# Optimization experiments

Measured on AMD Instinct MI355X. Metric: run time of the kernel, lower is better.

## Reference

```python
import jax, jax.numpy as jnp
import numpy as np


def sparse_conv3d(images, kernel, default_value, base_plane, dilations=(1, 1, 1)):
    """Sparse 3D conv over a per-pixel base-plane-aligned volume.

    images:     [B, H, W, D, C]  local depth slabs per pixel
    kernel:     [kh, kw, kd, C, F]
    base_plane: [B, H, W, 1] int  global depth offset of slab start per pixel
    Neighbor sample at pixel (h', w') and local depth d uses that neighbor's
    local index d + od + base_plane[h,w] - base_plane[h',w']; out-of-range
    (spatial or depth) samples are filled with default_value.
    """
    B, H, W, D, C = images.shape
    kh, kw, kd, _, F = kernel.shape
    d0, d1, d2 = dilations
    bp = base_plane[..., 0].astype(jnp.int32)  # [B,H,W]
    hs = jnp.arange(H)
    ws = jnp.arange(W)
    ds = jnp.arange(D)
    dv = jnp.asarray(default_value, images.dtype).reshape(())
    out = jnp.zeros((B, H, W, D, F), images.dtype)
    for i in range(kh):
        oh = (i - kh // 2) * d0
        h_idx = hs + oh
        valid_h = (h_idx >= 0) & (h_idx < H)
        h_c = jnp.clip(h_idx, 0, H - 1)
        for j in range(kw):
            ow = (j - kw // 2) * d1
            w_idx = ws + ow
            valid_w = (w_idx >= 0) & (w_idx < W)
            w_c = jnp.clip(w_idx, 0, W - 1)
            # gather shifted neighbor slabs and their base offsets
            img_n = images[:, h_c][:, :, w_c]      # [B,H,W,D,C]
            bp_n = bp[:, h_c][:, :, w_c]            # [B,H,W]
            rel = (bp - bp_n)[..., None]            # depth realignment [B,H,W,1]
            sp_valid = (valid_h[None, :, None, None] & valid_w[None, None, :, None])
            for k in range(kd):
                od = (k - kd // 2) * d2
                d_idx = ds[None, None, None, :] + od + rel  # [B,H,W,D]
                valid = sp_valid & (d_idx >= 0) & (d_idx < D)
                d_c = jnp.clip(d_idx, 0, D - 1)
                vals = jnp.take_along_axis(img_n, d_c[..., None], axis=3)  # [B,H,W,D,C]
                vals = jnp.where(valid[..., None], vals, dv)
                out = out + jnp.einsum('bhwdc,cf->bhwdf', vals, kernel[i, j, k])
    return out


def setup_inputs() -> dict:
    key = jax.random.key(0)
    k1, k2, k3 = jax.random.split(key, 3)
    B, H, W, D, C, F = 2, 96, 128, 32, 16, 16
    images = jax.random.normal(k1, (B, H, W, D, C), dtype=jnp.float32)
    base_plane = jax.random.randint(k2, (B, H, W, 1), 0, 8, dtype=jnp.int32)
    kernel = jax.random.normal(k3, (3, 3, 3, C, F), dtype=jnp.float32) * 0.05
    default_value = jnp.zeros((1,), dtype=jnp.float32)
    return {"images": images, "base_plane": base_plane, "kernel": kernel,
            "default_value": default_value}


def reference(images, base_plane, kernel, default_value):
    return sparse_conv3d(images, kernel, default_value[0], base_plane, dilations=(1, 1, 1))
```

## Files before the change

kernel.cpp:

```cpp
#include <hip/hip_runtime.h>
#include <hip/hip_bf16.h>

typedef __attribute__((ext_vector_type(8))) short short8;
typedef __attribute__((ext_vector_type(4))) short s16x4;
typedef __attribute__((ext_vector_type(4))) float f32x4;

#define NB_H 96
#define NB_W 128
#define NB_D 32
#define NB_C 16
#define NB_F 16
#define NPIX (2 * NB_H * NB_W)
#define KB2_U16 (14 * 512)
#define WS_NEED ((size_t)KB2_U16 * 2)
#define SLAB_STRIDE 1280
#define NSLAB 24
#define DV_OFF (NSLAB * SLAB_STRIDE)
#define LDS_BYTES (DV_OFF + 64)

static __device__ __forceinline__ short fcvt(float f) {
  return (short)__builtin_bit_cast(unsigned short, __float2bfloat16(f));
}


__global__ __launch_bounds__(256) void sconv3d_wprep(
    const float* __restrict__ kern, unsigned short* __restrict__ kb2) {
  const int i = blockIdx.x * 256 + threadIdx.x;
  if (i >= KB2_U16) return;
  const int p = i >> 9;
  const int g = (i >> 7) & 3;
  const int f = (i >> 3) & 15;
  const int j = i & 7;
  const int k = g * 8 + j;
  int lo, hi;
  if (p < 12) {
    const int q = p / 3, m = p % 3;
    lo = (m == 0) ? 6 * q : (m == 1) ? 6 * q + 3 : 6 * q + 2;
    hi = (m == 0) ? 6 * q + 1 : (m == 1) ? 6 * q + 4 : 6 * q + 5;
  } else if (p == 12) { lo = 24; hi = 25; }
  else { lo = 26; hi = -1; }
  const int t = (k < 16) ? lo : hi;
  const int c = k & 15;
  kb2[i] = (t >= 0) ? (unsigned short)fcvt(kern[(t * 16 + c) * 16 + f])
                    : (unsigned short)0;
}

__global__ __launch_bounds__(256, 4) void sconv3d_fused4(
    const float* __restrict__ img, const int* __restrict__ bp,
    const unsigned short* __restrict__ kb2, const float* __restrict__ dvp,
    float* __restrict__ out) {
  __shared__ char Sb[LDS_BYTES];
  const int tid = threadIdx.x;
  const int lane = tid & 63;
  const int r = lane & 15;
  const int grp = lane >> 4;
  const int vc = (grp & 1) * 16;
  const int halfbit = grp >> 1;
  const int rA = r + halfbit - 1;
  const int rX = r + 1;
  const int voff_dv = DV_OFF + vc;

  short8 bfrag[14];
#pragma unroll
  for (int p = 0; p < 14; ++p)
    bfrag[p] = *(const short8*)(kb2 + p * 512 + grp * 128 + r * 8);

  const int bid = (blockIdx.x & 7) * 384 + (blockIdx.x >> 3);
  const int b = bid >= 1536;
  const int rem = bid - b * 1536;
  const int h0 = (rem >> 5) * 2;
  const int w0 = (rem & 31) * 4;

  const int t2 = tid & 127;
  const int sg = tid >> 7;
  const int srow = t2 >> 2;
  const int sb8 = (t2 & 3) * 8;
#pragma unroll
  for (int pass = 0; pass < 12; ++pass) {
    const int s = pass * 2 + sg;
    const int dh = s / 6, dw = s - 6 * dh;
    const int hh = min(max(h0 + dh - 1, 0), NB_H - 1);
    const int ww = min(max(w0 + dw - 1, 0), NB_W - 1);
    const float4 v = *(const float4*)(
        img + ((b * NB_H + hh) * NB_W + ww) * (NB_D * NB_C) + t2 * 4);
    s16x4 o;
    o[0] = fcvt(v.x); o[1] = fcvt(v.y); o[2] = fcvt(v.z); o[3] = fcvt(v.w);
    *(s16x4*)(Sb + s * SLAB_STRIDE + srow * 40 + sb8) = o;
  }
  if (tid < 16) ((unsigned short*)(Sb + DV_OFF))[tid] =
      (unsigned short)fcvt(dvp[0]);

  const int wid = __builtin_amdgcn_readfirstlane((int)(tid >> 6));
  const int w = w0 + wid;
  const int hA = h0, hB = h0 + 1;
  const int pixA = (b * NB_H + hA) * NB_W + w;
  const int pixB = pixA + NB_W;
  const int bpcA = bp[pixA];
  const int bpcB = bp[pixB];

#define CALCN(PH, H, BPC, DI, DJ, SV, BA, RE)                           \
  {                                                                     \
    const int hh = (H) + (DI), ww = w + (DJ);                           \
    SV = (hh >= 0) & (hh < NB_H) & (ww >= 0) & (ww < NB_W);             \
    const int hc = min(max(hh, 0), NB_H - 1);                           \
    const int wc = min(max(ww, 0), NB_W - 1);                           \
    RE = (BPC)-bp[(b * NB_H + hc) * NB_W + wc];                         \
    BA = (((PH) + (DI) + 1) * 6 + wid + (DJ) + 1) * SLAB_STRIDE;        \
  }

  int Asv0, Aba0, Are0, Asv1, Aba1, Are1, Asv2, Aba2, Are2;
  int Asv3, Aba3, Are3, Asv4, Aba4, Are4, Asv5, Aba5, Are5;
  int Asv6, Aba6, Are6, Asv7, Aba7, Are7, Asv8, Aba8, Are8;
  int Bsv0, Bba0, Bre0, Bsv1, Bba1, Bre1, Bsv2, Bba2, Bre2;
  int Bsv3, Bba3, Bre3, Bsv4, Bba4, Bre4, Bsv5, Bba5, Bre5;
  int Bsv6, Bba6, Bre6, Bsv7, Bba7, Bre7, Bsv8, Bba8, Bre8;
  CALCN(0, hA, bpcA, -1, -1, Asv0, Aba0, Are0);
  CALCN(0, hA, bpcA, -1, 0, Asv1, Aba1, Are1);
  CALCN(0, hA, bpcA, -1, 1, Asv2, Aba2, Are2);
  CALCN(0, hA, bpcA, 0, -1, Asv3, Aba3, Are3);
  CALCN(0, hA, bpcA, 0, 0, Asv4, Aba4, Are4);
  CALCN(0, hA, bpcA, 0, 1, Asv5, Aba5, Are5);
  CALCN(0, hA, bpcA, 1, -1, Asv6, Aba6, Are6);
  CALCN(0, hA, bpcA, 1, 0, Asv7, Aba7, Are7);
  CALCN(0, hA, bpcA, 1, 1, Asv8, Aba8, Are8);
  CALCN(1, hB, bpcB, -1, -1, Bsv0, Bba0, Bre0);
  CALCN(1, hB, bpcB, -1, 0, Bsv1, Bba1, Bre1);
  CALCN(1, hB, bpcB, -1, 1, Bsv2, Bba2, Bre2);
  CALCN(1, hB, bpcB, 0, -1, Bsv3, Bba3, Bre3);
  CALCN(1, hB, bpcB, 0, 0, Bsv4, Bba4, Bre4);
  CALCN(1, hB, bpcB, 0, 1, Bsv5, Bba5, Bre5);
  CALCN(1, hB, bpcB, 1, -1, Bsv6, Bba6, Bre6);
  CALCN(1, hB, bpcB, 1, 0, Bsv7, Bba7, Bre7);
  CALCN(1, hB, bpcB, 1, 1, Bsv8, Bba8, Bre8);
#undef CALCN

  __syncthreads();

  f32x4 accA0 = {0.f, 0.f, 0.f, 0.f}, accA1 = {0.f, 0.f, 0.f, 0.f};
  f32x4 accB0 = {0.f, 0.f, 0.f, 0.f}, accB1 = {0.f, 0.f, 0.f, 0.f};

  short8 Xa0, Xa1, Xb0, Xb1, Ya0, Ya1, Yb0, Yb1;

#define LOADQ(S, DS0A, BAA, SVA, DS0B, BAB, SVB)                        \
  {                                                                     \
    int d_, o_;                                                         \
    d_ = (DS0A);      o_ = (BAA) + d_ * 40 + vc;                        \
    o_ = ((SVA) && (unsigned)d_ < NB_D) ? o_ : voff_dv;                 \
    S##a0 = *(const short8*)(Sb + o_);                                  \
    d_ = (DS0A) + 16; o_ = (BAA) + d_ * 40 + vc;                        \
    o_ = ((SVA) && (unsigned)d_ < NB_D) ? o_ : voff_dv;                 \
    S##a1 = *(const short8*)(Sb + o_);                                  \
    d_ = (DS0B);      o_ = (BAB) + d_ * 40 + vc;                        \
    o_ = ((SVB) && (unsigned)d_ < NB_D) ? o_ : voff_dv;                 \
    S##b0 = *(const short8*)(Sb + o_);                                  \
    d_ = (DS0B) + 16; o_ = (BAB) + d_ * 40 + vc;                        \
    o_ = ((SVB) && (unsigned)d_ < NB_D) ? o_ : voff_dv;                 \
    S##b1 = *(const short8*)(Sb + o_);                                  \
  }

#define LOAD_U(S, N) \
  LOADQ(S, rA + Are##N, Aba##N, Asv##N, rA + Bre##N, Bba##N, Bsv##N)

#define LOAD_M(S, NE, NO)                                               \
  {                                                                     \
    const int asv = halfbit ? Asv##NO : Asv##NE;                        \
    const int aba = halfbit ? Aba##NO : Aba##NE;                        \
    const int are = halfbit ? Are##NO : Are##NE;                        \
    const int bsv = halfbit ? Bsv##NO : Bsv##NE;                        \
    const int bba = halfbit ? Bba##NO : Bba##NE;                        \
    const int bre = halfbit ? Bre##NO : Bre##NE;                        \
    LOADQ(S, rX + are, aba, asv, rX + bre, bba, bsv)                    \
  }

#define LOAD_M13(S, NE)                                                 \
  {                                                                     \
    const int asv = halfbit ? 0 : Asv##NE;                              \
    const int bsv = halfbit ? 0 : Bsv##NE;                              \
    LOADQ(S, rX + Are##NE, Aba##NE, asv, rX + Bre##NE, Bba##NE, bsv)    \
  }

#define FMA4(P, S)                                                      \
  {                                                                     \
    const short8 bf = bfrag[P];                                         \
    accA0 = __builtin_amdgcn_mfma_f32_16x16x32_bf16(S##a0, bf, accA0, 0, 0, 0); \
    accA1 = __builtin_amdgcn_mfma_f32_16x16x32_bf16(S##a1, bf, accA1, 0, 0, 0); \
    accB0 = __builtin_amdgcn_mfma_f32_16x16x32_bf16(S##b0, bf, accB0, 0, 0, 0); \
    accB1 = __builtin_amdgcn_mfma_f32_16x16x32_bf16(S##b1, bf, accB1, 0, 0, 0); \
  }

  LOAD_U(X, 0);
  LOAD_U(Y, 1);
  FMA4(0, X);  LOAD_M(X, 0, 1);
  FMA4(1, Y);  LOAD_U(Y, 2);
  FMA4(2, X);  LOAD_U(X, 3);
  FMA4(3, Y);  LOAD_M(Y, 2, 3);
  FMA4(4, X);  LOAD_U(X, 4);
  FMA4(5, Y);  LOAD_U(Y, 5);
  FMA4(6, X);  LOAD_M(X, 4, 5);
  FMA4(7, Y);  LOAD_U(Y, 6);
  FMA4(8, X);  LOAD_U(X, 7);
  FMA4(9, Y);  LOAD_M(Y, 6, 7);
  FMA4(10, X); LOAD_U(X, 8);
  FMA4(11, Y); LOAD_M13(Y, 8);
  FMA4(12, X);
  FMA4(13, Y);

#undef LOADQ
#undef LOAD_U
#undef LOAD_M
#undef LOAD_M13
#undef FMA4

  const int obaseA = pixA * (NB_D * NB_F);
  const int obaseB = pixB * (NB_D * NB_F);
#pragma unroll
  for (int rr = 0; rr < 4; ++rr) {
    out[obaseA + (grp * 4 + rr) * NB_F + r] = accA0[rr];
    out[obaseA + (grp * 4 + rr + 16) * NB_F + r] = accA1[rr];
    out[obaseB + (grp * 4 + rr) * NB_F + r] = accB0[rr];
    out[obaseB + (grp * 4 + rr + 16) * NB_F + r] = accB1[rr];
  }
}

__global__ __launch_bounds__(256) void sconv3d_mfma(
    const float* __restrict__ img, const int* __restrict__ bp,
    const float* __restrict__ kern, const float* __restrict__ dvp,
    float* __restrict__ out, int npix) {
  __shared__ unsigned short Kb[28 * 256];
  const int tid = threadIdx.x;
  for (int idx = tid; idx < 28 * 256; idx += 256) {
    unsigned short v = 0;
    if (idx < 27 * 256) v = (unsigned short)fcvt(kern[idx]);
    Kb[idx] = v;
  }
  __syncthreads();

  const int lane = tid & 63;
  const int grp = lane >> 4;
  const int r = lane & 15;
  const int c0 = (grp & 1) * 8;
  const int half = grp >> 1;

  short8 bfrag[14];
#pragma unroll
  for (int p = 0; p < 14; ++p) {
#pragma unroll
    for (int j = 0; j < 8; ++j) {
      const int k = 8 * grp + j;
      const int t = 2 * p + (k >> 4);
      bfrag[p][j] = (short)Kb[t * 256 + (k & 15) * 16 + r];
    }
  }

  const int pix = blockIdx.x * 4 + (tid >> 6);
  if (pix >= npix) return;
  const int b = pix / (NB_H * NB_W);
  const int rem = pix - b * (NB_H * NB_W);
  const int h = rem >> 7;
  const int w = rem & (NB_W - 1);

  const float dv = dvp[0];
  const int bpc = bp[pix];

  f32x4 acc0 = {0.f, 0.f, 0.f, 0.f};
  f32x4 acc1 = {0.f, 0.f, 0.f, 0.f};

#pragma unroll
  for (int p = 0; p < 14; ++p) {
    const int t = 2 * p + half;
    const int n = t / 3;
    const int kd = t - 3 * n;
    const int i = n / 3;
    const int j = n - 3 * i;
    const int hh = h + i - 1;
    const int ww = w + j - 1;
    const bool sv =
        (t < 27) && (hh >= 0) && (hh < NB_H) && (ww >= 0) && (ww < NB_W);
    const int hc = min(max(hh, 0), NB_H - 1);
    const int wc = min(max(ww, 0), NB_W - 1);
    const int nidx = (b * NB_H + hc) * NB_W + wc;
    const int rel = bpc - bp[nidx];
    const int base = nidx * (NB_D * NB_C);
    const int dsh = (kd - 1) + rel;

    const int ds0 = r + dsh;
    short8 a0;
    {
      float va[8];
      if (sv && (ds0 >= 0) && (ds0 < NB_D)) {
        const float4* pp = (const float4*)(img + base + ds0 * NB_C + c0);
        const float4 x = pp[0];
        const float4 y = pp[1];
        va[0] = x.x; va[1] = x.y; va[2] = x.z; va[3] = x.w;
        va[4] = y.x; va[5] = y.y; va[6] = y.z; va[7] = y.w;
      } else {
#pragma unroll
        for (int q = 0; q < 8; ++q) va[q] = dv;
      }
#pragma unroll
      for (int q = 0; q < 8; ++q) a0[q] = fcvt(va[q]);
    }
    acc0 = __builtin_amdgcn_mfma_f32_16x16x32_bf16(a0, bfrag[p], acc0, 0, 0, 0);

    const int ds1 = ds0 + 16;
    short8 a1;
    {
      float va[8];
      if (sv && (ds1 >= 0) && (ds1 < NB_D)) {
        const float4* pp = (const float4*)(img + base + ds1 * NB_C + c0);
        const float4 x = pp[0];
        const float4 y = pp[1];
        va[0] = x.x; va[1] = x.y; va[2] = x.z; va[3] = x.w;
        va[4] = y.x; va[5] = y.y; va[6] = y.z; va[7] = y.w;
      } else {
#pragma unroll
        for (int q = 0; q < 8; ++q) va[q] = dv;
      }
#pragma unroll
      for (int q = 0; q < 8; ++q) a1[q] = fcvt(va[q]);
    }
    acc1 = __builtin_amdgcn_mfma_f32_16x16x32_bf16(a1, bfrag[p], acc1, 0, 0, 0);
  }

  const int obase = pix * (NB_D * NB_F);
#pragma unroll
  for (int rr = 0; rr < 4; ++rr) {
    out[obase + (grp * 4 + rr) * NB_F + r] = acc0[rr];
    out[obase + (grp * 4 + rr + 16) * NB_F + r] = acc1[rr];
  }
}

extern "C" void kernel_launch(void* const* d_in, const int* in_sizes, int n_in,
                              void* d_out, int out_size, void* d_ws, size_t ws_size,
                              hipStream_t stream) {
  const float* img = (const float*)d_in[0];
  const int* bp = (const int*)d_in[1];
  const float* kern = (const float*)d_in[2];
  const float* dvp = (const float*)d_in[3];
  float* out = (float*)d_out;

  if (ws_size >= WS_NEED) {
    unsigned short* kb2 = (unsigned short*)d_ws;
    sconv3d_wprep<<<28, 256, 0, stream>>>(kern, kb2);
    sconv3d_fused4<<<NPIX / 8, 256, 0, stream>>>(img, bp, kb2, dvp, out);
  } else {
    sconv3d_mfma<<<NPIX / 4, 256, 0, stream>>>(img, bp, kern, dvp, out, NPIX);
  }
}
```

Measured before the change: 47.17 us.

## Roll a six-row LDS ring buffer so each block sweeps twelve output rows

Each block now covers a 12x4 pixel strip instead of 2x4. It keeps a rolling ring of six halo rows of bf16 slabs in LDS, and each step prefetches the next two rows into registers, overlapping those loads with the MFMA work on the current two rows. This cuts the redundant halo reloads from global memory (previously 24 slabs per 8 pixels) and spreads the weight-fragment setup over more work. In exchange the grid shrinks to 512 blocks with a larger LDS footprint and occupancy hint 2, there is a barrier per step, and there are fewer blocks to hide latency across CUs.

After: 51.81 us. 1.1x slower.

```diff
diff --git a/kernel.cpp b/kernel.cpp
--- a/kernel.cpp
+++ b/kernel.cpp
@@ -14,7 +14,7 @@
 #define KB2_U16 (14 * 512)
 #define WS_NEED ((size_t)KB2_U16 * 2)
 #define SLAB_STRIDE 1280
-#define NSLAB 24
+#define NSLAB 36
 #define DV_OFF (NSLAB * SLAB_STRIDE)
 #define LDS_BYTES (DV_OFF + 64)
 
@@ -45,7 +45,7 @@
                     : (unsigned short)0;
 }
 
-__global__ __launch_bounds__(256, 4) void sconv3d_fused4(
+__global__ __launch_bounds__(256, 2) void sconv3d_roll(
     const float* __restrict__ img, const int* __restrict__ bp,
     const unsigned short* __restrict__ kb2, const float* __restrict__ dvp,
     float* __restrict__ out) {
@@ -65,81 +65,112 @@
   for (int p = 0; p < 14; ++p)
     bfrag[p] = *(const short8*)(kb2 + p * 512 + grp * 128 + r * 8);
 
-  const int bid = (blockIdx.x & 7) * 384 + (blockIdx.x >> 3);
-  const int b = bid >= 1536;
-  const int rem = bid - b * 1536;
-  const int h0 = (rem >> 5) * 2;
+  const int bid = (blockIdx.x & 7) * 64 + (blockIdx.x >> 3);
+  const int b = bid >= 256;
+  const int rem = bid - b * 256;
+  const int h0 = (rem >> 5) * 12;
   const int w0 = (rem & 31) * 4;
 
+  const int sg = tid >> 7;
   const int t2 = tid & 127;
-  const int sg = tid >> 7;
-  const int srow = t2 >> 2;
-  const int sb8 = (t2 & 3) * 8;
-#pragma unroll
-  for (int pass = 0; pass < 12; ++pass) {
-    const int s = pass * 2 + sg;
-    const int dh = s / 6, dw = s - 6 * dh;
-    const int hh = min(max(h0 + dh - 1, 0), NB_H - 1);
-    const int ww = min(max(w0 + dw - 1, 0), NB_W - 1);
+  const int drow = t2 >> 2;
+  const int sq8 = (t2 & 3) * 8;
+
+#pragma unroll
+  for (int k = 0; k < 12; ++k) {
+    const int r2 = 2 * k + sg;
+    const int row = r2 / 6;
+    const int col = r2 - 6 * row;
+    const int hr = h0 - 1 + row;
+    const int hh = min(max(hr, 0), NB_H - 1);
+    const int ww = min(max(w0 + col - 1, 0), NB_W - 1);
     const float4 v = *(const float4*)(
         img + ((b * NB_H + hh) * NB_W + ww) * (NB_D * NB_C) + t2 * 4);
     s16x4 o;
     o[0] = fcvt(v.x); o[1] = fcvt(v.y); o[2] = fcvt(v.z); o[3] = fcvt(v.w);
-    *(s16x4*)(Sb + s * SLAB_STRIDE + srow * 40 + sb8) = o;
+    const int slot = (hr - h0 + 1) % 6;
+    *(s16x4*)(Sb + (slot * 6 + col) * SLAB_STRIDE + drow * 40 + sq8) = o;
   }
   if (tid < 16) ((unsigned short*)(Sb + DV_OFF))[tid] =
       (unsigned short)fcvt(dvp[0]);
 
   const int wid = __builtin_amdgcn_readfirstlane((int)(tid >> 6));
   const int w = w0 + wid;
-  const int hA = h0, hB = h0 + 1;
-  const int pixA = (b * NB_H + hA) * NB_W + w;
-  const int pixB = pixA + NB_W;
-  const int bpcA = bp[pixA];
-  const int bpcB = bp[pixB];
-
-#define CALCN(PH, H, BPC, DI, DJ, SV, BA, RE)                           \
-  {                                                                     \
-    const int hh = (H) + (DI), ww = w + (DJ);                           \
+
+#pragma unroll
+  for (int p = 0; p < 14; ++p)
+    asm volatile("" : "+v"(bfrag[p]));
+
+  __syncthreads();
+
+#pragma unroll 1
+  for (int j = 0; j < 6; ++j) {
+    const int h = h0 + 2 * j;
+
+    float4 stv[6];
+    int stb[6];
+    if (j < 5) {
+#pragma unroll
+      for (int k = 0; k < 6; ++k) {
+        const int r2 = 2 * k + sg;
+        const int row = (r2 >= 6) ? 1 : 0;
+        const int col = r2 - 6 * row;
+        const int hr = h + 3 + row;
+        const int hh = min(hr, NB_H - 1);
+        const int ww = min(max(w0 + col - 1, 0), NB_W - 1);
+        stv[k] = *(const float4*)(
+            img + ((b * NB_H + hh) * NB_W + ww) * (NB_D * NB_C) + t2 * 4);
+        stb[k] = (((hr - h0 + 1) % 6) * 6 + col) * SLAB_STRIDE +
+                 drow * 40 + sq8;
+      }
+    }
+
+    const int pixA = (b * NB_H + h) * NB_W + w;
+    const int pixB = pixA + NB_W;
+    const int bpcA = bp[pixA];
+    const int bpcB = bp[pixB];
+
+#define CALCN(HROW, BPC, DI, DJ, SV, BA, RE)                            \
+  {                                                                     \
+    const int hh = (HROW) + (DI), ww = w + (DJ);                        \
     SV = (hh >= 0) & (hh < NB_H) & (ww >= 0) & (ww < NB_W);             \
     const int hc = min(max(hh, 0), NB_H - 1);                           \
     const int wc = min(max(ww, 0), NB_W - 1);                           \
     RE = (BPC)-bp[(b * NB_H + hc) * NB_W + wc];                         \
-    BA = (((PH) + (DI) + 1) * 6 + wid + (DJ) + 1) * SLAB_STRIDE;        \
-  }
-
-  int Asv0, Aba0, Are0, Asv1, Aba1, Are1, Asv2, Aba2, Are2;
-  int Asv3, Aba3, Are3, Asv4, Aba4, Are4, Asv5, Aba5, Are5;
-  int Asv6, Aba6, Are6, Asv7, Aba7, Are7, Asv8, Aba8, Are8;
-  int Bsv0, Bba0, Bre0, Bsv1, Bba1, Bre1, Bsv2, Bba2, Bre2;
-  int Bsv3, Bba3, Bre3, Bsv4, Bba4, Bre4, Bsv5, Bba5, Bre5;
-  int Bsv6, Bba6, Bre6, Bsv7, Bba7, Bre7, Bsv8, Bba8, Bre8;
-  CALCN(0, hA, bpcA, -1, -1, Asv0, Aba0, Are0);
-  CALCN(0, hA, bpcA, -1, 0, Asv1, Aba1, Are1);
-  CALCN(0, hA, bpcA, -1, 1, Asv2, Aba2, Are2);
-  CALCN(0, hA, bpcA, 0, -1, Asv3, Aba3, Are3);
-  CALCN(0, hA, bpcA, 0, 0, Asv4, Aba4, Are4);
-  CALCN(0, hA, bpcA, 0, 1, Asv5, Aba5, Are5);
-  CALCN(0, hA, bpcA, 1, -1, Asv6, Aba6, Are6);
-  CALCN(0, hA, bpcA, 1, 0, Asv7, Aba7, Are7);
-  CALCN(0, hA, bpcA, 1, 1, Asv8, Aba8, Are8);
-  CALCN(1, hB, bpcB, -1, -1, Bsv0, Bba0, Bre0);
-  CALCN(1, hB, bpcB, -1, 0, Bsv1, Bba1, Bre1);
-  CALCN(1, hB, bpcB, -1, 1, Bsv2, Bba2, Bre2);
-  CALCN(1, hB, bpcB, 0, -1, Bsv3, Bba3, Bre3);
-  CALCN(1, hB, bpcB, 0, 0, Bsv4, Bba4, Bre4);
-  CALCN(1, hB, bpcB, 0, 1, Bsv5, Bba5, Bre5);
-  CALCN(1, hB, bpcB, 1, -1, Bsv6, Bba6, Bre6);
-  CALCN(1, hB, bpcB, 1, 0, Bsv7, Bba7, Bre7);
-  CALCN(1, hB, bpcB, 1, 1, Bsv8, Bba8, Bre8);
+    BA = ((((HROW)-h0 + (DI) + 1) % 6) * 6 + wid + (DJ) + 1) *          \
+         SLAB_STRIDE;                                                   \
+  }
+
+    int Asv0, Aba0, Are0, Asv1, Aba1, Are1, Asv2, Aba2, Are2;
+    int Asv3, Aba3, Are3, Asv4, Aba4, Are4, Asv5, Aba5, Are5;
+    int Asv6, Aba6, Are6, Asv7, Aba7, Are7, Asv8, Aba8, Are8;
+    int Bsv0, Bba0, Bre0, Bsv1, Bba1, Bre1, Bsv2, Bba2, Bre2;
+    int Bsv3, Bba3, Bre3, Bsv4, Bba4, Bre4, Bsv5, Bba5, Bre5;
+    int Bsv6, Bba6, Bre6, Bsv7, Bba7, Bre7, Bsv8, Bba8, Bre8;
+    CALCN(h, bpcA, -1, -1, Asv0, Aba0, Are0);
+    CALCN(h, bpcA, -1, 0, Asv1, Aba1, Are1);
+    CALCN(h, bpcA, -1, 1, Asv2, Aba2, Are2);
+    CALCN(h, bpcA, 0, -1, Asv3, Aba3, Are3);
+    CALCN(h, bpcA, 0, 0, Asv4, Aba4, Are4);
+    CALCN(h, bpcA, 0, 1, Asv5, Aba5, Are5);
+    CALCN(h, bpcA, 1, -1, Asv6, Aba6, Are6);
+    CALCN(h, bpcA, 1, 0, Asv7, Aba7, Are7);
+    CALCN(h, bpcA, 1, 1, Asv8, Aba8, Are8);
+    CALCN(h + 1, bpcB, -1, -1, Bsv0, Bba0, Bre0);
+    CALCN(h + 1, bpcB, -1, 0, Bsv1, Bba1, Bre1);
+    CALCN(h + 1, bpcB, -1, 1, Bsv2, Bba2, Bre2);
+    CALCN(h + 1, bpcB, 0, -1, Bsv3, Bba3, Bre3);
+    CALCN(h + 1, bpcB, 0, 0, Bsv4, Bba4, Bre4);
+    CALCN(h + 1, bpcB, 0, 1, Bsv5, Bba5, Bre5);
+    CALCN(h + 1, bpcB, 1, -1, Bsv6, Bba6, Bre6);
+    CALCN(h + 1, bpcB, 1, 0, Bsv7, Bba7, Bre7);
+    CALCN(h + 1, bpcB, 1, 1, Bsv8, Bba8, Bre8);
 #undef CALCN
 
-  __syncthreads();
-
-  f32x4 accA0 = {0.f, 0.f, 0.f, 0.f}, accA1 = {0.f, 0.f, 0.f, 0.f};
-  f32x4 accB0 = {0.f, 0.f, 0.f, 0.f}, accB1 = {0.f, 0.f, 0.f, 0.f};
-
-  short8 Xa0, Xa1, Xb0, Xb1, Ya0, Ya1, Yb0, Yb1;
+    f32x4 accA0 = {0.f, 0.f, 0.f, 0.f}, accA1 = {0.f, 0.f, 0.f, 0.f};
+    f32x4 accB0 = {0.f, 0.f, 0.f, 0.f}, accB1 = {0.f, 0.f, 0.f, 0.f};
+
+    short8 Xa0, Xa1, Xb0, Xb1, Ya0, Ya1, Yb0, Yb1;
 
 #define LOADQ(S, DS0A, BAA, SVA, DS0B, BAB, SVB)                        \
   {                                                                     \
@@ -188,22 +219,22 @@
     accB1 = __builtin_amdgcn_mfma_f32_16x16x32_bf16(S##b1, bf, accB1, 0, 0, 0); \
   }
 
-  LOAD_U(X, 0);
-  LOAD_U(Y, 1);
-  FMA4(0, X);  LOAD_M(X, 0, 1);
-  FMA4(1, Y);  LOAD_U(Y, 2);
-  FMA4(2, X);  LOAD_U(X, 3);
-  FMA4(3, Y);  LOAD_M(Y, 2, 3);
-  FMA4(4, X);  LOAD_U(X, 4);
-  FMA4(5, Y);  LOAD_U(Y, 5);
-  FMA4(6, X);  LOAD_M(X, 4, 5);
-  FMA4(7, Y);  LOAD_U(Y, 6);
-  FMA4(8, X);  LOAD_U(X, 7);
-  FMA4(9, Y);  LOAD_M(Y, 6, 7);
-  FMA4(10, X); LOAD_U(X, 8);
-  FMA4(11, Y); LOAD_M13(Y, 8);
-  FMA4(12, X);
-  FMA4(13, Y);
+    LOAD_U(X, 0);
+    LOAD_U(Y, 1);
+    FMA4(0, X);  LOAD_M(X, 0, 1);
+    FMA4(1, Y);  LOAD_U(Y, 2);
+    FMA4(2, X);  LOAD_U(X, 3);
+    FMA4(3, Y);  LOAD_M(Y, 2, 3);
+    FMA4(4, X);  LOAD_U(X, 4);
+    FMA4(5, Y);  LOAD_U(Y, 5);
+    FMA4(6, X);  LOAD_M(X, 4, 5);
+    FMA4(7, Y);  LOAD_U(Y, 6);
+    FMA4(8, X);  LOAD_U(X, 7);
+    FMA4(9, Y);  LOAD_M(Y, 6, 7);
+    FMA4(10, X); LOAD_U(X, 8);
+    FMA4(11, Y); LOAD_M13(Y, 8);
+    FMA4(12, X);
+    FMA4(13, Y);
 
 #undef LOADQ
 #undef LOAD_U
@@ -211,14 +242,26 @@
 #undef LOAD_M13
 #undef FMA4
 
-  const int obaseA = pixA * (NB_D * NB_F);
-  const int obaseB = pixB * (NB_D * NB_F);
-#pragma unroll
-  for (int rr = 0; rr < 4; ++rr) {
-    out[obaseA + (grp * 4 + rr) * NB_F + r] = accA0[rr];
-    out[obaseA + (grp * 4 + rr + 16) * NB_F + r] = accA1[rr];
-    out[obaseB + (grp * 4 + rr) * NB_F + r] = accB0[rr];
-    out[obaseB + (grp * 4 + rr + 16) * NB_F + r] = accB1[rr];
+    const int obaseA = pixA * (NB_D * NB_F);
+    const int obaseB = pixB * (NB_D * NB_F);
+#pragma unroll
+    for (int rr = 0; rr < 4; ++rr) {
+      out[obaseA + (grp * 4 + rr) * NB_F + r] = accA0[rr];
+      out[obaseA + (grp * 4 + rr + 16) * NB_F + r] = accA1[rr];
+      out[obaseB + (grp * 4 + rr) * NB_F + r] = accB0[rr];
+      out[obaseB + (grp * 4 + rr + 16) * NB_F + r] = accB1[rr];
+    }
+
+    if (j < 5) {
+#pragma unroll
+      for (int k = 0; k < 6; ++k) {
+        s16x4 o;
+        o[0] = fcvt(stv[k].x); o[1] = fcvt(stv[k].y);
+        o[2] = fcvt(stv[k].z); o[3] = fcvt(stv[k].w);
+        *(s16x4*)(Sb + stb[k]) = o;
+      }
+    }
+    __syncthreads();
   }
 }
 
@@ -342,7 +385,7 @@
   if (ws_size >= WS_NEED) {
     unsigned short* kb2 = (unsigned short*)d_ws;
     sconv3d_wprep<<<28, 256, 0, stream>>>(kern, kb2);
-    sconv3d_fused4<<<NPIX / 8, 256, 0, stream>>>(img, bp, kb2, dvp, out);
+    sconv3d_roll<<<512, 256, 0, stream>>>(img, bp, kb2, dvp, out);
   } else {
     sconv3d_mfma<<<NPIX / 4, 256, 0, stream>>>(img, bp, kern, dvp, out, NPIX);
   }
```

## Pre-convert images to padded bf16 workspace and stage via global_load_lds

Applied to the files above, without the earlier changes.

A prep kernel now converts the whole fp32 image into a padded bf16 slab layout in the workspace, alongside the weight prep. The main kernel then copies those slabs and the weight fragments straight into LDS with async global_load_lds, instead of converting fp32 in registers. Weight fragments are read from LDS per MFMA group rather than held in 14 registers. The aim is to cut the main kernel's halo reload traffic and register pressure. The cost is an extra full pass that reads the image and writes a padded copy, and the workspace requirement grows.

Result: slower. 54.13 us (+14.8%).

```diff
diff --git a/kernel.cpp b/kernel.cpp
--- a/kernel.cpp
+++ b/kernel.cpp
@@ -11,44 +11,77 @@
 #define NB_C 16
 #define NB_F 16
 #define NPIX (2 * NB_H * NB_W)
+#define SLAB_STRIDE 1280
+#define IMGPAD ((size_t)NPIX * SLAB_STRIDE)
 #define KB2_U16 (14 * 512)
-#define WS_NEED ((size_t)KB2_U16 * 2)
-#define SLAB_STRIDE 1280
+#define WS_NEED (IMGPAD + (size_t)KB2_U16 * 2)
 #define NSLAB 24
 #define DV_OFF (NSLAB * SLAB_STRIDE)
-#define LDS_BYTES (DV_OFF + 64)
+#define KB_OFF (DV_OFF + 64)
+#define LDS_BYTES (KB_OFF + KB2_U16 * 2)
 
 static __device__ __forceinline__ short fcvt(float f) {
   return (short)__builtin_bit_cast(unsigned short, __float2bfloat16(f));
 }
 
-
-__global__ __launch_bounds__(256) void sconv3d_wprep(
-    const float* __restrict__ kern, unsigned short* __restrict__ kb2) {
-  const int i = blockIdx.x * 256 + threadIdx.x;
-  if (i >= KB2_U16) return;
-  const int p = i >> 9;
-  const int g = (i >> 7) & 3;
-  const int f = (i >> 3) & 15;
-  const int j = i & 7;
-  const int k = g * 8 + j;
-  int lo, hi;
-  if (p < 12) {
-    const int q = p / 3, m = p % 3;
-    lo = (m == 0) ? 6 * q : (m == 1) ? 6 * q + 3 : 6 * q + 2;
-    hi = (m == 0) ? 6 * q + 1 : (m == 1) ? 6 * q + 4 : 6 * q + 5;
-  } else if (p == 12) { lo = 24; hi = 25; }
-  else { lo = 26; hi = -1; }
-  const int t = (k < 16) ? lo : hi;
-  const int c = k & 15;
-  kb2[i] = (t >= 0) ? (unsigned short)fcvt(kern[(t * 16 + c) * 16 + f])
-                    : (unsigned short)0;
-}
-
-__global__ __launch_bounds__(256, 4) void sconv3d_fused4(
-    const float* __restrict__ img, const int* __restrict__ bp,
-    const unsigned short* __restrict__ kb2, const float* __restrict__ dvp,
-    float* __restrict__ out) {
+static __device__ __forceinline__ void gl_lds16(const void* g, void* l) {
+  __builtin_amdgcn_global_load_lds(
+      (const __attribute__((address_space(1))) unsigned int*)g,
+      (__attribute__((address_space(3))) unsigned int*)l, 16, 0, 0);
+}
+static __device__ __forceinline__ void gl_lds4(const void* g, void* l) {
+  __builtin_amdgcn_global_load_lds(
+      (const __attribute__((address_space(1))) unsigned int*)g,
+      (__attribute__((address_space(3))) unsigned int*)l, 4, 0, 0);
+}
+
+
+__global__ __launch_bounds__(256) void sconv3d_prep(
+    const float* __restrict__ img, const float* __restrict__ kern,
+    char* __restrict__ wsc) {
+  const int tid = threadIdx.x;
+  if (blockIdx.x < NPIX / 16) {
+    const int pix = blockIdx.x * 16 + (tid >> 4);
+    const int j = tid & 15;
+    const float* src = img + (size_t)pix * (NB_D * NB_C);
+    char* dst = wsc + (size_t)pix * SLAB_STRIDE;
+#pragma unroll
+    for (int k = 0; k < 10; ++k) {
+      const int c = j + k * 16;
+      const int row = c / 5, cc = c - 5 * row;
+      s16x4 o = {0, 0, 0, 0};
+      if (cc < 4) {
+        const float4 v = *(const float4*)(src + row * 16 + cc * 4);
+        o[0] = fcvt(v.x); o[1] = fcvt(v.y);
+        o[2] = fcvt(v.z); o[3] = fcvt(v.w);
+      }
+      *(s16x4*)(dst + c * 8) = o;
+    }
+  } else {
+    const int i = (blockIdx.x - NPIX / 16) * 256 + tid;
+    const int p = i >> 9;
+    const int g = (i >> 7) & 3;
+    const int f = (i >> 3) & 15;
+    const int jj = i & 7;
+    const int k = g * 8 + jj;
+    int lo, hi;
+    if (p < 12) {
+      const int q = p / 3, m = p % 3;
+      lo = (m == 0) ? 6 * q : (m == 1) ? 6 * q + 3 : 6 * q + 2;
+      hi = (m == 0) ? 6 * q + 1 : (m == 1) ? 6 * q + 4 : 6 * q + 5;
+    } else if (p == 12) { lo = 24; hi = 25; }
+    else { lo = 26; hi = -1; }
+    const int t = (k < 16) ? lo : hi;
+    const int c = k & 15;
+    ((unsigned short*)(wsc + IMGPAD))[i] =
+        (t >= 0) ? (unsigned short)fcvt(kern[(t * 16 + c) * 16 + f])
+                 : (unsigned short)0;
+  }
+}
+
+__global__ __launch_bounds__(256, 4) void sconv3d_glds(
+    const char* __restrict__ wsc, const int* __restrict__ bp,
+    const float* __restrict__ dvp, float* __restrict__ out) {
   __shared__ char Sb[LDS_BYTES];
   const int tid = threadIdx.x;
   const int lane = tid & 63;
@@ -60,52 +93,48 @@
   const int rX = r + 1;
   const int voff_dv = DV_OFF + vc;
 
-  short8 bfrag[14];
-#pragma unroll
-  for (int p = 0; p < 14; ++p)
-    bfrag[p] = *(const short8*)(kb2 + p * 512 + grp * 128 + r * 8);
-
   const int bid = (blockIdx.x & 7) * 384 + (blockIdx.x >> 3);
   const int b = bid >= 1536;
   const int rem = bid - b * 1536;
   const int h0 = (rem >> 5) * 2;
   const int w0 = (rem & 31) * 4;
 
-  const int t2 = tid & 127;
-  const int sg = tid >> 7;
-  const int srow = t2 >> 2;
-  const int sb8 = (t2 & 3) * 8;
-#pragma unroll
-  for (int pass = 0; pass < 12; ++pass) {
-    const int s = pass * 2 + sg;
-    const int dh = s / 6, dw = s - 6 * dh;
-    const int hh = min(max(h0 + dh - 1, 0), NB_H - 1);
-    const int ww = min(max(w0 + dw - 1, 0), NB_W - 1);
-    const float4 v = *(const float4*)(
-        img + ((b * NB_H + hh) * NB_W + ww) * (NB_D * NB_C) + t2 * 4);
-    s16x4 o;
-    o[0] = fcvt(v.x); o[1] = fcvt(v.y); o[2] = fcvt(v.z); o[3] = fcvt(v.w);
-    *(s16x4*)(Sb + s * SLAB_STRIDE + srow * 40 + sb8) = o;
-  }
-  if (tid < 16) ((unsigned short*)(Sb + DV_OFF))[tid] =
-      (unsigned short)fcvt(dvp[0]);
-
-  const int wid = __builtin_amdgcn_readfirstlane((int)(tid >> 6));
-  const int w = w0 + wid;
-  const int hA = h0, hB = h0 + 1;
-  const int pixA = (b * NB_H + hA) * NB_W + w;
+  const int wk = __builtin_amdgcn_readfirstlane((int)(tid >> 6));
+
+  {
+    const int hh = min(max(h0 + wk - 1, 0), NB_H - 1);
+#pragma unroll
+    for (int dw = 0; dw < 6; ++dw) {
+      const int ww = min(max(w0 + dw - 1, 0), NB_W - 1);
+      const int nidx = (b * NB_H + hh) * NB_W + ww;
+      const char* src = wsc + (size_t)nidx * SLAB_STRIDE;
+      char* dst = Sb + (wk * 6 + dw) * SLAB_STRIDE;
+      gl_lds16(src + lane * 16, dst);
+      gl_lds4(src + 1024 + lane * 4, dst + 1024);
+    }
+#pragma unroll
+    for (int i = 0; i < 4; ++i) {
+      const int idx = wk + 4 * i;
+      if (idx < 14)
+        gl_lds16(wsc + IMGPAD + idx * 1024 + lane * 16, Sb + KB_OFF + idx * 1024);
+    }
+  }
+  const float dvf = dvp[0];
+
+  const int w = w0 + wk;
+  const int pixA = (b * NB_H + h0) * NB_W + w;
   const int pixB = pixA + NB_W;
   const int bpcA = bp[pixA];
   const int bpcB = bp[pixB];
 
-#define CALCN(PH, H, BPC, DI, DJ, SV, BA, RE)                           \
-  {                                                                     \
-    const int hh = (H) + (DI), ww = w + (DJ);                           \
+#define CALCN(PH, BPC, DI, DJ, SV, BA, RE)                              \
+  {                                                                     \
+    const int hh = h0 + (PH) + (DI), ww = w + (DJ);                     \
     SV = (hh >= 0) & (hh < NB_H) & (ww >= 0) & (ww < NB_W);             \
     const int hc = min(max(hh, 0), NB_H - 1);                           \
     const int wc = min(max(ww, 0), NB_W - 1);                           \
     RE = (BPC)-bp[(b * NB_H + hc) * NB_W + wc];                         \
-    BA = (((PH) + (DI) + 1) * 6 + wid + (DJ) + 1) * SLAB_STRIDE;        \
+    BA = (((PH) + (DI) + 1) * 6 + wk + (DJ) + 1) * SLAB_STRIDE;         \
   }
 
   int Asv0, Aba0, Are0, Asv1, Aba1, Are1, Asv2, Aba2, Are2;
@@ -114,25 +143,28 @@
   int Bsv0, Bba0, Bre0, Bsv1, Bba1, Bre1, Bsv2, Bba2, Bre2;
   int Bsv3, Bba3, Bre3, Bsv4, Bba4, Bre4, Bsv5, Bba5, Bre5;
   int Bsv6, Bba6, Bre6, Bsv7, Bba7, Bre7, Bsv8, Bba8, Bre8;
-  CALCN(0, hA, bpcA, -1, -1, Asv0, Aba0, Are0);
-  CALCN(0, hA, bpcA, -1, 0, Asv1, Aba1, Are1);
-  CALCN(0, hA, bpcA, -1, 1, Asv2, Aba2, Are2);
-  CALCN(0, hA, bpcA, 0, -1, Asv3, Aba3, Are3);
-  CALCN(0, hA, bpcA, 0, 0, Asv4, Aba4, Are4);
-  CALCN(0, hA, bpcA, 0, 1, Asv5, Aba5, Are5);
-  CALCN(0, hA, bpcA, 1, -1, Asv6, Aba6, Are6);
-  CALCN(0, hA, bpcA, 1, 0, Asv7, Aba7, Are7);
-  CALCN(0, hA, bpcA, 1, 1, Asv8, Aba8, Are8);
-  CALCN(1, hB, bpcB, -1, -1, Bsv0, Bba0, Bre0);
-  CALCN(1, hB, bpcB, -1, 0, Bsv1, Bba1, Bre1);
-  CALCN(1, hB, bpcB, -1, 1, Bsv2, Bba2, Bre2);
-  CALCN(1, hB, bpcB, 0, -1, Bsv3, Bba3, Bre3);
-  CALCN(1, hB, bpcB, 0, 0, Bsv4, Bba4, Bre4);
-  CALCN(1, hB, bpcB, 0, 1, Bsv5, Bba5, Bre5);
-  CALCN(1, hB, bpcB, 1, -1, Bsv6, Bba6, Bre6);
-  CALCN(1, hB, bpcB, 1, 0, Bsv7, Bba7, Bre7);
-  CALCN(1, hB, bpcB, 1, 1, Bsv8, Bba8, Bre8);
+  CALCN(0, bpcA, -1, -1, Asv0, Aba0, Are0);
+  CALCN(0, bpcA, -1, 0, Asv1, Aba1, Are1);
+  CALCN(0, bpcA, -1, 1, Asv2, Aba2, Are2);
+  CALCN(0, bpcA, 0, -1, Asv3, Aba3, Are3);
+  CALCN(0, bpcA, 0, 0, Asv4, Aba4, Are4);
+  CALCN(0, bpcA, 0, 1, Asv5, Aba5, Are5);
+  CALCN(0, bpcA, 1, -1, Asv6, Aba6, Are6);
+  CALCN(0, bpcA, 1, 0, Asv7, Aba7, Are7);
+  CALCN(0, bpcA, 1, 1, Asv8, Aba8, Are8);
+  CALCN(1, bpcB, -1, -1, Bsv0, Bba0, Bre0);
+  CALCN(1, bpcB, -1, 0, Bsv1, Bba1, Bre1);
+  CALCN(1, bpcB, -1, 1, Bsv2, Bba2, Bre2);
+  CALCN(1, bpcB, 0, -1, Bsv3, Bba3, Bre3);
+  CALCN(1, bpcB, 0, 0, Bsv4, Bba4, Bre4);
+  CALCN(1, bpcB, 0, 1, Bsv5, Bba5, Bre5);
+  CALCN(1, bpcB, 1, -1, Bsv6, Bba6, Bre6);
+  CALCN(1, bpcB, 1, 0, Bsv7, Bba7, Bre7);
+  CALCN(1, bpcB, 1, 1, Bsv8, Bba8, Bre8);
 #undef CALCN
+
+  if (tid < 16) ((unsigned short*)(Sb + DV_OFF))[tid] =
+      (unsigned short)fcvt(dvf);
 
   __syncthreads();
 
@@ -181,11 +213,12 @@
 
 #define FMA4(P, S)                                                      \
   {                                                                     \
-    const short8 bf = bfrag[P];                                         \
-    accA0 = __builtin_amdgcn_mfma_f32_16x16x32_bf16(S##a0, bf, accA0, 0, 0, 0); \
-    accA1 = __builtin_amdgcn_mfma_f32_16x16x32_bf16(S##a1, bf, accA1, 0, 0, 0); \
-    accB0 = __builtin_amdgcn_mfma_f32_16x16x32_bf16(S##b0, bf, accB0, 0, 0, 0); \
-    accB1 = __builtin_amdgcn_mfma_f32_16x16x32_bf16(S##b1, bf, accB1, 0, 0, 0); \
+    const short8 bfv = *(const short8*)(Sb + KB_OFF + (P) * 1024 +      \
+                                        grp * 256 + r * 16);            \
+    accA0 = __builtin_amdgcn_mfma_f32_16x16x32_bf16(S##a0, bfv, accA0, 0, 0, 0); \
+    accA1 = __builtin_amdgcn_mfma_f32_16x16x32_bf16(S##a1, bfv, accA1, 0, 0, 0); \
+    accB0 = __builtin_amdgcn_mfma_f32_16x16x32_bf16(S##b0, bfv, accB0, 0, 0, 0); \
+    accB1 = __builtin_amdgcn_mfma_f32_16x16x32_bf16(S##b1, bfv, accB1, 0, 0, 0); \
   }
 
   LOAD_U(X, 0);
@@ -295,10 +328,10 @@
         va[4] = y.x; va[5] = y.y; va[6] = y.z; va[7] = y.w;
       } else {
 #pragma unroll
-        for (int q = 0; q < 8; ++q) va[q] = dv;
+        for (int qq = 0; qq < 8; ++qq) va[qq] = dv;
       }
 #pragma unroll
-      for (int q = 0; q < 8; ++q) a0[q] = fcvt(va[q]);
+      for (int qq = 0; qq < 8; ++qq) a0[qq] = fcvt(va[qq]);
     }
     acc0 = __builtin_amdgcn_mfma_f32_16x16x32_bf16(a0, bfrag[p], acc0, 0, 0, 0);
 
@@ -314,10 +347,10 @@
         va[4] = y.x; va[5] = y.y; va[6] = y.z; va[7] = y.w;
       } else {
 #pragma unroll
-        for (int q = 0; q < 8; ++q) va[q] = dv;
+        for (int qq = 0; qq < 8; ++qq) va[qq] = dv;
       }
 #pragma unroll
-      for (int q = 0; q < 8; ++q) a1[q] = fcvt(va[q]);
+      for (int qq = 0; qq < 8; ++qq) a1[qq] = fcvt(va[qq]);
     }
     acc1 = __builtin_amdgcn_mfma_f32_16x16x32_bf16(a1, bfrag[p], acc1, 0, 0, 0);
   }
@@ -340,9 +373,9 @@
   float* out = (float*)d_out;
 
   if (ws_size >= WS_NEED) {
-    unsigned short* kb2 = (unsigned short*)d_ws;
-    sconv3d_wprep<<<28, 256, 0, stream>>>(kern, kb2);
-    sconv3d_fused4<<<NPIX / 8, 256, 0, stream>>>(img, bp, kb2, dvp, out);
+    char* wsc = (char*)d_ws;
+    sconv3d_prep<<<NPIX / 16 + 28, 256, 0, stream>>>(img, kern, wsc);
+    sconv3d_glds<<<NPIX / 8, 256, 0, stream>>>(wsc, bp, dvp, out);
   } else {
     sconv3d_mfma<<<NPIX / 4, 256, 0, stream>>>(img, bp, kern, dvp, out, NPIX);
   }
```
